# Kernel optimization log

Measured on AMD Instinct MI355X. Metric: run time of the kernel, lower is better.

## Reference

```python
import jax, jax.numpy as jnp
import numpy as np

N_EMBED = 1024
N_HEAD = 16
BLOCK_SIZE = 2048
ROPE_BASE = 10000.0


def _rope_cache():
    # theta uses n_embed (full model dim) as denominator, as in the source,
    # then is truncated to head_size//2 frequencies.
    hs_half = N_EMBED // N_HEAD // 2
    j = jnp.arange(N_EMBED // 2, dtype=jnp.float32)
    theta = jnp.power(ROPE_BASE, -2.0 * j / N_EMBED)
    seq_idx = jnp.arange(BLOCK_SIZE, dtype=jnp.float32)
    idx_theta = jnp.einsum('i,j->ij', seq_idx, theta)[:, :hs_half]  # [block, hs/2]
    return jnp.stack([jnp.cos(idx_theta), jnp.sin(idx_theta)], axis=-1)  # [block, hs/2, 2]


def _apply_rope(x, cache):
    # x: [B, nh, T, hs]. FAITHFUL to source: rope indexes its cache by dim-1,
    # which here is the HEAD dim (rope is called after transpose(1,2)).
    B, d1, d2, hs = x.shape
    rc = cache[:d1, :hs // 2]            # [d1, hs/2, 2]
    rc = rc[None, :, None, :, :]          # [1, d1, 1, hs/2, 2]
    x2 = x.reshape(B, d1, d2, hs // 2, 2)
    cos, sin = rc[..., 0], rc[..., 1]
    xr, xi = x2[..., 0], x2[..., 1]
    rot = jnp.stack([xr * cos - xi * sin, xi * cos + xr * sin], axis=-1)
    return rot.reshape(B, d1, d2, hs).astype(x.dtype)


def setup_inputs() -> dict:
    key = jax.random.key(0)
    ks = jax.random.split(key, 5)
    B, T, C = 2, 2048, N_EMBED
    return {
        'x': jax.random.normal(ks[0], (B, T, C), dtype=jnp.float32),
        'w_attn': jax.random.normal(ks[1], (C, 3 * C), dtype=jnp.float32) * 0.02,
        'b_attn': jax.random.normal(ks[2], (3 * C,), dtype=jnp.float32) * 0.02,
        'w_proj': jax.random.normal(ks[3], (C, C), dtype=jnp.float32) * 0.02,
        'b_proj': jax.random.normal(ks[4], (C,), dtype=jnp.float32) * 0.02,
    }


def reference(x, w_attn, b_attn, w_proj, b_proj):
    B, T, C = x.shape
    nh, hs = N_HEAD, C // N_HEAD
    qkv = x @ w_attn + b_attn                     # [B, T, 3C]
    q, k, v = jnp.split(qkv, 3, axis=-1)
    q = q.reshape(B, T, nh, hs).transpose(0, 2, 1, 3)  # [B, nh, T, hs]
    k = k.reshape(B, T, nh, hs).transpose(0, 2, 1, 3)
    v = v.reshape(B, T, nh, hs).transpose(0, 2, 1, 3)
    cache = _rope_cache()
    q = _apply_rope(q, cache)
    k = _apply_rope(k, cache)
    scale = 1.0 / jnp.sqrt(jnp.asarray(hs, dtype=q.dtype))
    scores = jnp.einsum('bhqd,bhkd->bhqk', q, k) * scale
    causal = jnp.tril(jnp.ones((T, T), dtype=bool))
    scores = jnp.where(causal[None, None], scores, jnp.finfo(scores.dtype).min)
    attn = jax.nn.softmax(scores, axis=-1)
    y = jnp.einsum('bhqk,bhkd->bhqd', attn, v)    # [B, nh, T, hs]
    y = y.transpose(0, 2, 1, 3).reshape(B, T, C)
    return y @ w_proj + b_proj
```

## Files before the change

### kernel.cpp

```cpp
#include <hip/hip_runtime.h>
#include <hip/hip_bf16.h>
#include <math.h>

#define TSEQ 2048
#define CEMB 1024
#define NHEAD 16
#define HS 64

typedef __attribute__((ext_vector_type(8))) short bf16x8;
typedef __attribute__((ext_vector_type(4))) float f32x4;
typedef __attribute__((ext_vector_type(16))) float f32x16;
typedef unsigned int u32;
typedef unsigned long long u64;
typedef unsigned short u16;

__device__ __forceinline__ void gload16(const void* g, void* l) {
    __builtin_amdgcn_global_load_lds(
        (const __attribute__((address_space(1))) unsigned int*)g,
        (__attribute__((address_space(3))) unsigned int*)l, 16, 0, 0);
}

__device__ __forceinline__ u32 pk2(float a, float b) {
    union { u32 u; __hip_bfloat16 h[2]; } t;
    t.h[0] = __float2bfloat16(a); t.h[1] = __float2bfloat16(b);
    return t.u;
}

__device__ __forceinline__ u16 bf16u(float a) {
    union { u16 u; __hip_bfloat16 h; } t;
    t.h = __float2bfloat16(a);
    return t.u;
}

__device__ const int UNIT_TBL[24] = {22,7,20,21,19,17,6,14,
                                     23,18,16,12,4,5,13,15,
                                     0,1,2,3,10,8,9,11};

__device__ __forceinline__ void transpose_tile(const float* __restrict__ src,
                                               __hip_bfloat16* __restrict__ dst,
                                               int K, int N, int n0, int k0) {
    __shared__ float tile[32][33];
    int tx = threadIdx.x & 31, ty = threadIdx.x >> 5;
#pragma unroll
    for (int i = 0; i < 32; i += 8)
        tile[ty + i][tx] = src[(size_t)(k0 + ty + i) * N + n0 + tx];
    __syncthreads();
#pragma unroll
    for (int i = 0; i < 32; i += 8)
        dst[(size_t)(n0 + ty + i) * K + k0 + tx] = __float2bfloat16(tile[tx][ty + i]);
}

__global__ __launch_bounds__(256) void prep_k(
    const float* __restrict__ x, __hip_bfloat16* __restrict__ Xb,
    float* __restrict__ tbl,
    const float* __restrict__ w_attn, __hip_bfloat16* __restrict__ Wta,
    const float* __restrict__ w_proj, __hip_bfloat16* __restrict__ Wpt)
{
    const int id = blockIdx.x;
    if (id < 2048) {
        int i = (id * 256 + threadIdx.x) * 8;
        float4 a = *(const float4*)(x + i);
        float4 b = *(const float4*)(x + i + 4);
        union { bf16x8 v; __hip_bfloat16 h[8]; } pk;
        pk.h[0] = __float2bfloat16(a.x); pk.h[1] = __float2bfloat16(a.y);
        pk.h[2] = __float2bfloat16(a.z); pk.h[3] = __float2bfloat16(a.w);
        pk.h[4] = __float2bfloat16(b.x); pk.h[5] = __float2bfloat16(b.y);
        pk.h[6] = __float2bfloat16(b.z); pk.h[7] = __float2bfloat16(b.w);
        *(bf16x8*)(Xb + i) = pk.v;
    } else if (id == 2048) {
#pragma unroll
        for (int it = 0; it < 2; ++it) {
            int idx = threadIdx.x + 256 * it;
            int h = idx >> 5, j = idx & 31;
            double theta = pow(10000.0, -2.0 * (double)j / 1024.0);
            double ang = (double)h * theta;
            tbl[2 * idx + 0] = (float)cos(ang);
            tbl[2 * idx + 1] = (float)sin(ang);
        }
    } else if (id < 2049 + 3072) {
        int t = id - 2049;
        transpose_tile(w_attn, Wta, CEMB, 3 * CEMB, (t % 96) * 32, (t / 96) * 32);
    } else {
        int t = id - (2049 + 3072);
        transpose_tile(w_proj, Wpt, CEMB, CEMB, (t & 31) * 32, (t >> 5) * 32);
    }
}

__global__ __launch_bounds__(256) void qkv_mfma_k(
    const __hip_bfloat16* __restrict__ Xb, const __hip_bfloat16* __restrict__ Wt,
    const float* __restrict__ bias, const float* __restrict__ tbl,
    __hip_bfloat16* __restrict__ Qb, __hip_bfloat16* __restrict__ Kb,
    __hip_bfloat16* __restrict__ Vtb)
{
    __shared__ __hip_bfloat16 SM[4][128 * 32];
    const int tid = threadIdx.x;
    const int lane = tid & 63, w = tid >> 6;
    const int lr = lane & 15, lg = lane >> 4;
    const int wm = w >> 1, wn = w & 1;
    const int n0 = blockIdx.x * 128;
    const int m0 = blockIdx.y * 128;
    const __hip_bfloat16* gA = Xb + (size_t)(m0 + (tid >> 2)) * CEMB + (tid & 3) * 8;
    const __hip_bfloat16* gB = Wt + (size_t)(n0 + (tid >> 2)) * CEMB + (tid & 3) * 8;
#define QSTAGE(buf, kk) do { \
        gload16(gA + (kk), &SM[buf][tid * 8]); \
        gload16(gA + 64 * CEMB + (kk), &SM[buf][2048 + tid * 8]); \
        gload16(gB + (kk), &SM[2 + (buf)][tid * 8]); \
        gload16(gB + 64 * CEMB + (kk), &SM[2 + (buf)][2048 + tid * 8]); } while (0)
    f32x4 acc[4][4] = {};
    QSTAGE(0, 0);
    __syncthreads();
    for (int k0 = 0; k0 < CEMB; k0 += 32) {
        const int cur = (k0 >> 5) & 1;
        if (k0 + 32 < CEMB) QSTAGE(cur ^ 1, k0 + 32);
        bf16x8 af[4], bfr[4];
#pragma unroll
        for (int mi = 0; mi < 4; ++mi)
            af[mi] = *(const bf16x8*)&SM[cur][(wm * 64 + mi * 16 + lr) * 32 + lg * 8];
#pragma unroll
        for (int ni = 0; ni < 4; ++ni)
            bfr[ni] = *(const bf16x8*)&SM[2 + cur][(wn * 64 + ni * 16 + lr) * 32 + lg * 8];
#pragma unroll
        for (int mi = 0; mi < 4; ++mi)
#pragma unroll
            for (int ni = 0; ni < 4; ++ni)
                acc[mi][ni] = __builtin_amdgcn_mfma_f32_16x16x32_bf16(af[mi], bfr[ni], acc[mi][ni], 0, 0, 0);
        __syncthreads();
    }
    const int sec = (n0 >> 10);
    const int bb = m0 >> 11;
    const int t0v = m0 & 2047;
    const int h0 = (n0 & 1023) >> 6;
    if (sec == 2) {
        char* T = (char*)SM;
#pragma unroll
        for (int mi = 0; mi < 4; ++mi) {
#pragma unroll
            for (int ni = 0; ni < 4; ++ni) {
                const int nl = wn * 64 + ni * 16 + lr;
                const float bv = bias[n0 + nl];
                const int mb = wm * 64 + mi * 16 + lg * 4;
                union { u64 u; __hip_bfloat16 hh[4]; } pk;
#pragma unroll
                for (int r = 0; r < 4; ++r) pk.hh[r] = __float2bfloat16(acc[mi][ni][r] + bv);
                *(u64*)(T + nl * 256 + ((mb * 2) ^ ((nl & 7) << 4))) = pk.u;
            }
        }
        __syncthreads();
#pragma unroll
        for (int i = 0; i < 8; ++i) {
            int cid = tid + 256 * i;
            int n = cid >> 4, mc = cid & 15;
            bf16x8 v = *(const bf16x8*)(T + n * 256 + ((mc * 16) ^ ((n & 7) << 4)));
            *(bf16x8*)&Vtb[(((size_t)bb * NHEAD + h0 + (n >> 6)) * HS + (n & 63)) * TSEQ + t0v + mc * 8] = v;
        }
    } else {
        char* T = (char*)SM;
        const float sc = (sec == 0) ? 0.18033688011112042f : 1.0f;
        __hip_bfloat16* dst = (sec == 0) ? Qb : Kb;
#pragma unroll
        for (int mi = 0; mi < 4; ++mi) {
#pragma unroll
            for (int ni = 0; ni < 4; ++ni) {
                const int nl = wn * 64 + ni * 16 + lr;
                const int c63 = (n0 + nl) & 63;
                const int h = h0 + (nl >> 6);
                const int j = c63 >> 1;
                const float cth = tbl[(h * 32 + j) * 2 + 0];
                const float sth = tbl[(h * 32 + j) * 2 + 1];
                const float bv = bias[n0 + nl];
                const int mb = wm * 64 + mi * 16 + lg * 4;
#pragma unroll
                for (int r = 0; r < 4; ++r) {
                    float val = acc[mi][ni][r] + bv;
                    float prt = __shfl_xor(val, 1);
                    float rot = (lr & 1) ? (val * cth + prt * sth) : (val * cth - prt * sth);
                    const int row = mb + r;
                    *(u16*)(T + row * 256 + ((nl * 2) ^ ((row & 7) << 4))) = bf16u(rot * sc);
                }
            }
        }
        __syncthreads();
#pragma unroll
        for (int i = 0; i < 8; ++i) {
            int cid = tid + 256 * i;
            int row = cid >> 4, nc = cid & 15;
            bf16x8 v = *(const bf16x8*)(T + row * 256 + ((nc * 16) ^ ((row & 7) << 4)));
            int col = nc * 8;
            *(bf16x8*)&dst[(((size_t)bb * NHEAD + h0 + (col >> 6)) * TSEQ + t0v + row) * HS + (col & 63)] = v;
        }
    }
#undef QSTAGE
}

__global__ __launch_bounds__(256) void attn_split_k(
    const __hip_bfloat16* __restrict__ Q, const __hip_bfloat16* __restrict__ K,
    const __hip_bfloat16* __restrict__ Vt, __hip_bfloat16* __restrict__ Y,
    __hip_bfloat16* __restrict__ Op, float* __restrict__ Mp, float* __restrict__ Lp)
{
    __shared__ __hip_bfloat16 KsBuf[2][64 * 64];
    __shared__ __hip_bfloat16 VsBuf[2][64 * 64];
    const int tid = threadIdx.x;
    const int w = tid >> 6;
    const int lane = tid & 63;
    const int l31 = lane & 31;
    const int hi = lane >> 5;
    const int id = blockIdx.x;
    const int bh = id & 31;
    const int u = UNIT_TBL[id >> 5];
    int qbb, kt0, ktN, half;
    bool split;
    if (u < 8) { qbb = u; half = 0; kt0 = 0; ktN = 2 * u + 2; split = false; }
    else {
        qbb = 8 + ((u - 8) >> 1); half = (u - 8) & 1;
        kt0 = half ? (qbb + 1) : 0;
        ktN = half ? (2 * qbb + 2) : (qbb + 1);
        split = true;
    }
    const size_t bho = (size_t)bh * TSEQ * HS;
    const int Qw = qbb * 128 + w * 32;

    int srcK[2], srcV[2];
#pragma unroll
    for (int j = 0; j < 2; ++j) {
        int L = (tid + 256 * j) * 16;
        int row = L >> 7;
        int ce = ((L & 127) ^ (((row ^ (row >> 3)) & 7) << 4)) >> 1;
        srcK[j] = row * HS + ce;
        srcV[j] = row * TSEQ + ce;
    }
    const __hip_bfloat16* Kg = K + bho;
    const __hip_bfloat16* Vg = Vt + bho;
#define ASTAGE(buf, kt_) do { \
        const __hip_bfloat16* kg_ = Kg + (size_t)(kt_) * 64 * HS; \
        const __hip_bfloat16* vg_ = Vg + (size_t)(kt_) * 64; \
        char* kb_ = (char*)KsBuf[buf]; char* vb_ = (char*)VsBuf[buf]; \
        _Pragma("unroll") \
        for (int j = 0; j < 2; ++j) { \
            gload16(kg_ + srcK[j], kb_ + (tid + 256 * j) * 16); \
            gload16(vg_ + srcV[j], vb_ + (tid + 256 * j) * 16); } } while (0)

    bf16x8 qf[4];
    {
        const __hip_bfloat16* qp = Q + bho + (size_t)(Qw + l31) * HS + hi * 8;
#pragma unroll
        for (int kb = 0; kb < 4; ++kb) qf[kb] = *(const bf16x8*)(qp + kb * 16);
    }
    const int base0 = l31 * 128;
    const int swz0 = ((l31 ^ (l31 >> 3)) & 7) << 4;
    const int r32 = 32 + l31;
    const int base1 = r32 * 128;
    const int swz1 = ((r32 ^ (r32 >> 3)) & 7) << 4;

    float mrow = -1e30f, lsum = 0.f;
    f32x16 o0 = {}, o1 = {};

    ASTAGE(0, kt0);
    __syncthreads();
    for (int kt = kt0; kt < ktN; ++kt) {
        const int cur = (kt - kt0) & 1;
        if (kt + 1 < ktN) ASTAGE(cur ^ 1, kt + 1);
        const char* KsB = (const char*)KsBuf[cur];
        const char* VsB = (const char*)VsBuf[cur];
        const int kvb0 = kt * 64, kvb1 = kt * 64 + 32;
        const bool do0 = kvb0 <= Qw;
        const bool do1 = kvb1 <= Qw;
        if (do0) {
            f32x16 s0 = {}, s1 = {};
            __builtin_amdgcn_s_setprio(1);
#pragma unroll
            for (int kb = 0; kb < 4; ++kb) {
                bf16x8 kf = *(const bf16x8*)(KsB + base0 + ((kb * 32 + hi * 16) ^ swz0));
                s0 = __builtin_amdgcn_mfma_f32_32x32x16_bf16(kf, qf[kb], s0, 0, 0, 0);
            }
            if (do1) {
#pragma unroll
                for (int kb = 0; kb < 4; ++kb) {
                    bf16x8 kf = *(const bf16x8*)(KsB + base1 + ((kb * 32 + hi * 16) ^ swz1));
                    s1 = __builtin_amdgcn_mfma_f32_32x32x16_bf16(kf, qf[kb], s1, 0, 0, 0);
                }
            }
            __builtin_amdgcn_s_setprio(0);
            if (kvb0 == Qw) {
#pragma unroll
                for (int r = 0; r < 16; ++r) {
                    int crow = (r & 3) + 8 * (r >> 2) + 4 * hi;
                    if (crow > l31) s0[r] = -1e30f;
                }
            }
            if (do1 && kvb1 == Qw) {
#pragma unroll
                for (int r = 0; r < 16; ++r) {
                    int crow = (r & 3) + 8 * (r >> 2) + 4 * hi;
                    if (crow > l31) s1[r] = -1e30f;
                }
            }
            float mx = s0[0];
#pragma unroll
            for (int r = 1; r < 16; ++r) mx = fmaxf(mx, s0[r]);
            if (do1) {
#pragma unroll
                for (int r = 0; r < 16; ++r) mx = fmaxf(mx, s1[r]);
            }
            mx = fmaxf(mx, __shfl_xor(mx, 32));
            const float mn = fmaxf(mrow, mx);
            const float alpha = __builtin_amdgcn_exp2f(mrow - mn);
            mrow = mn;
            float ls = 0.f;
#pragma unroll
            for (int r = 0; r < 16; ++r) { s0[r] = __builtin_amdgcn_exp2f(s0[r] - mn); ls += s0[r]; }
            if (do1) {
#pragma unroll
                for (int r = 0; r < 16; ++r) { s1[r] = __builtin_amdgcn_exp2f(s1[r] - mn); ls += s1[r]; }
            }
            ls += __shfl_xor(ls, 32);
            lsum = lsum * alpha + ls;
            o0 = o0 * alpha;
            o1 = o1 * alpha;
            union { u32 u[4]; bf16x8 v; } pa[4];
            {
                u32 w01 = pk2(s0[0], s0[1]),   w23 = pk2(s0[2], s0[3]);
                u32 w45 = pk2(s0[4], s0[5]),   w67 = pk2(s0[6], s0[7]);
                u32 w89 = pk2(s0[8], s0[9]),   wab = pk2(s0[10], s0[11]);
                u32 wcd = pk2(s0[12], s0[13]), wef = pk2(s0[14], s0[15]);
                u32 xa = __shfl_xor(hi ? w01 : w45, 32);
                u32 xb = __shfl_xor(hi ? w23 : w67, 32);
                u32 xc = __shfl_xor(hi ? w89 : wcd, 32);
                u32 xd = __shfl_xor(hi ? wab : wef, 32);
                if (hi == 0) {
                    pa[0].u[0] = w01; pa[0].u[1] = w23; pa[0].u[2] = xa;  pa[0].u[3] = xb;
                    pa[1].u[0] = w89; pa[1].u[1] = wab; pa[1].u[2] = xc;  pa[1].u[3] = xd;
                } else {
                    pa[0].u[0] = xa;  pa[0].u[1] = xb;  pa[0].u[2] = w45; pa[0].u[3] = w67;
                    pa[1].u[0] = xc;  pa[1].u[1] = xd;  pa[1].u[2] = wcd; pa[1].u[3] = wef;
                }
            }
            if (do1) {
                u32 w01 = pk2(s1[0], s1[1]),   w23 = pk2(s1[2], s1[3]);
                u32 w45 = pk2(s1[4], s1[5]),   w67 = pk2(s1[6], s1[7]);
                u32 w89 = pk2(s1[8], s1[9]),   wab = pk2(s1[10], s1[11]);
                u32 wcd = pk2(s1[12], s1[13]), wef = pk2(s1[14], s1[15]);
                u32 xa = __shfl_xor(hi ? w01 : w45, 32);
                u32 xb = __shfl_xor(hi ? w23 : w67, 32);
                u32 xc = __shfl_xor(hi ? w89 : wcd, 32);
                u32 xd = __shfl_xor(hi ? wab : wef, 32);
                if (hi == 0) {
                    pa[2].u[0] = w01; pa[2].u[1] = w23; pa[2].u[2] = xa;  pa[2].u[3] = xb;
                    pa[3].u[0] = w89; pa[3].u[1] = wab; pa[3].u[2] = xc;  pa[3].u[3] = xd;
                } else {
                    pa[2].u[0] = xa;  pa[2].u[1] = xb;  pa[2].u[2] = w45; pa[2].u[3] = w67;
                    pa[3].u[0] = xc;  pa[3].u[1] = xd;  pa[3].u[2] = wcd; pa[3].u[3] = wef;
                }
            }
            __builtin_amdgcn_s_setprio(1);
#define PVC(ks) do { \
                bf16x8 vf0 = *(const bf16x8*)(VsB + base0 + (((ks) * 32 + hi * 16) ^ swz0)); \
                o0 = __builtin_amdgcn_mfma_f32_32x32x16_bf16(vf0, pa[ks].v, o0, 0, 0, 0); \
                bf16x8 vf1 = *(const bf16x8*)(VsB + base1 + (((ks) * 32 + hi * 16) ^ swz1)); \
                o1 = __builtin_amdgcn_mfma_f32_32x32x16_bf16(vf1, pa[ks].v, o1, 0, 0, 0); } while (0)
            PVC(0); PVC(1);
            if (do1) { PVC(2); PVC(3); }
#undef PVC
            __builtin_amdgcn_s_setprio(0);
        }
        __syncthreads();
    }
    if (!split) {
        char* T = (char*)KsBuf + w * 4096;
        const float inv = 1.f / lsum;
        const int tsw = (l31 & 7) << 4;
        const int tbase = l31 * 128;
#pragma unroll
        for (int r = 0; r < 16; ++r) {
            int d0 = (r & 3) + 8 * (r >> 2) + 4 * hi;
            *(__hip_bfloat16*)(T + tbase + ((d0 * 2) ^ tsw)) = __float2bfloat16(o0[r] * inv);
            *(__hip_bfloat16*)(T + tbase + (((d0 + 32) * 2) ^ tsw)) = __float2bfloat16(o1[r] * inv);
        }
        const int b = bh >> 4, h = bh & 15;
#pragma unroll
        for (int p = 0; p < 4; ++p) {
            int q = p * 8 + (lane >> 3);
            int colb = ((lane & 7) * 16) ^ ((q & 7) << 4);
            bf16x8 v = *(const bf16x8*)(T + q * 128 + colb);
            *(bf16x8*)(Y + ((size_t)b * TSEQ + Qw + q) * CEMB + h * HS + (lane & 7) * 8) = v;
        }
    } else {
        const int p = bh * 16 + (qbb - 8) * 2 + half;
        __hip_bfloat16* Ob = Op + (size_t)p * 8192;
        const int qloc = w * 32 + l31;
#pragma unroll
        for (int r = 0; r < 16; ++r) {
            int d0 = (r & 3) + 8 * (r >> 2) + 4 * hi;
            Ob[d0 * 128 + qloc] = __float2bfloat16(o0[r]);
            Ob[(d0 + 32) * 128 + qloc] = __float2bfloat16(o1[r]);
        }
        if (hi == 0) {
            Mp[p * 128 + qloc] = mrow;
            Lp[p * 128 + qloc] = lsum;
        }
    }
#undef ASTAGE
}

__global__ __launch_bounds__(256) void merge_k(
    const __hip_bfloat16* __restrict__ Op, const float* __restrict__ Mp,
    const float* __restrict__ Lp, __hip_bfloat16* __restrict__ Y)
{
    const int blk = blockIdx.x;
    const int bh = blk & 31, qq = blk >> 5;
    const int p0 = bh * 16 + qq * 2, p1 = p0 + 1;
    const int t = threadIdx.x;
    const int q = t >> 1, dg = (t & 1) * 32;
    const float m0 = Mp[p0 * 128 + q], m1 = Mp[p1 * 128 + q];
    const float l0 = Lp[p0 * 128 + q], l1 = Lp[p1 * 128 + q];
    const float m = fmaxf(m0, m1);
    const float w0 = exp2f(m0 - m), w1 = exp2f(m1 - m);
    const float inv = 1.f / (l0 * w0 + l1 * w1);
    const __hip_bfloat16* O0 = Op + (size_t)p0 * 8192;
    const __hip_bfloat16* O1 = Op + (size_t)p1 * 8192;
    union { bf16x8 v[4]; __hip_bfloat16 h[32]; } outp;
#pragma unroll
    for (int i = 0; i < 32; ++i) {
        int d = dg + i;
        float a = __bfloat162float(O0[d * 128 + q]);
        float b = __bfloat162float(O1[d * 128 + q]);
        outp.h[i] = __float2bfloat16((a * w0 + b * w1) * inv);
    }
    const int b2 = bh >> 4, h = bh & 15;
    const int qg = (8 + qq) * 128 + q;
    __hip_bfloat16* yp = Y + ((size_t)b2 * TSEQ + qg) * CEMB + h * HS + dg;
#pragma unroll
    for (int i = 0; i < 4; ++i) *(bf16x8*)(yp + i * 8) = outp.v[i];
}

__global__ __launch_bounds__(256) void proj_mfma_k(
    const __hip_bfloat16* __restrict__ Ab, const __hip_bfloat16* __restrict__ Wt,
    const float* __restrict__ bias, float* __restrict__ out)
{
    __shared__ __hip_bfloat16 Al[2][128 * 32];
    __shared__ __hip_bfloat16 Bl[2][64 * 32];
    const int tid = threadIdx.x;
    const int lane = tid & 63, w = tid >> 6;
    const int lr = lane & 15, lg = lane >> 4;
    const int wm = w >> 1, wn = w & 1;
    const int n0 = blockIdx.x * 64;
    const int m0 = blockIdx.y * 128;
    const __hip_bfloat16* gA = Ab + (size_t)(m0 + (tid >> 2)) * CEMB + (tid & 3) * 8;
    const __hip_bfloat16* gB = Wt + (size_t)(n0 + (tid >> 2)) * CEMB + (tid & 3) * 8;
#define PSTAGE(buf, kk) do { \
        gload16(gA + (kk), &Al[buf][tid * 8]); \
        gload16(gA + 64 * CEMB + (kk), &Al[buf][2048 + tid * 8]); \
        gload16(gB + (kk), &Bl[buf][tid * 8]); } while (0)
    f32x4 acc[4][2] = {};
    PSTAGE(0, 0);
    __syncthreads();
    for (int k0 = 0; k0 < CEMB; k0 += 32) {
        const int cur = (k0 >> 5) & 1;
        if (k0 + 32 < CEMB) PSTAGE(cur ^ 1, k0 + 32);
        bf16x8 af[4], bfr[2];
#pragma unroll
        for (int mi = 0; mi < 4; ++mi)
            af[mi] = *(const bf16x8*)&Al[cur][(wm * 64 + mi * 16 + lr) * 32 + lg * 8];
#pragma unroll
        for (int ni = 0; ni < 2; ++ni)
            bfr[ni] = *(const bf16x8*)&Bl[cur][(wn * 32 + ni * 16 + lr) * 32 + lg * 8];
#pragma unroll
        for (int mi = 0; mi < 4; ++mi)
#pragma unroll
            for (int ni = 0; ni < 2; ++ni)
                acc[mi][ni] = __builtin_amdgcn_mfma_f32_16x16x32_bf16(af[mi], bfr[ni], acc[mi][ni], 0, 0, 0);
        __syncthreads();
    }
#pragma unroll
    for (int mi = 0; mi < 4; ++mi) {
#pragma unroll
        for (int ni = 0; ni < 2; ++ni) {
            const int gcol = n0 + wn * 32 + ni * 16 + lr;
            const float bv = bias[gcol];
            const int growb = m0 + wm * 64 + mi * 16 + lg * 4;
#pragma unroll
            for (int r = 0; r < 4; ++r)
                out[(size_t)(growb + r) * CEMB + gcol] = acc[mi][ni][r] + bv;
        }
    }
#undef PSTAGE
}

extern "C" void kernel_launch(void* const* d_in, const int* in_sizes, int n_in,
                              void* d_out, int out_size, void* d_ws, size_t ws_size,
                              hipStream_t stream)
{
    const float* x      = (const float*)d_in[0];
    const float* w_attn = (const float*)d_in[1];
    const float* b_attn = (const float*)d_in[2];
    const float* w_proj = (const float*)d_in[3];
    const float* b_proj = (const float*)d_in[4];
    float* out = (float*)d_out;
    char* base = (char*)d_ws;

    const size_t MB = 1048576;
    float* tbl          = (float*)base;
    __hip_bfloat16* Xb  = (__hip_bfloat16*)(base + 4096);
    __hip_bfloat16* Wta = (__hip_bfloat16*)(base + 4096 + 8 * MB);
    __hip_bfloat16* Wpt = (__hip_bfloat16*)(base + 4096 + 14 * MB);
    __hip_bfloat16* Qb  = (__hip_bfloat16*)(base + 4096 + 16 * MB);
    __hip_bfloat16* Kb  = (__hip_bfloat16*)(base + 4096 + 24 * MB);
    __hip_bfloat16* Vtb = (__hip_bfloat16*)(base + 4096 + 32 * MB);
    __hip_bfloat16* Yb  = Xb;
    const size_t PART_OFF = 4096 + 40 * MB;
    __hip_bfloat16* Op = (__hip_bfloat16*)(base + PART_OFF);
    float* Mp = (float*)(base + PART_OFF + 8 * MB);
    float* Lp = Mp + (size_t)512 * 128;

    prep_k<<<6145, 256, 0, stream>>>(x, Xb, tbl, w_attn, Wta, w_proj, Wpt);
    qkv_mfma_k<<<dim3(24, 32), 256, 0, stream>>>(Xb, Wta, b_attn, tbl, Qb, Kb, Vtb);
    attn_split_k<<<768, 256, 0, stream>>>(Qb, Kb, Vtb, Yb, Op, Mp, Lp);
    merge_k<<<256, 256, 0, stream>>>(Op, Mp, Lp, Yb);
    proj_mfma_k<<<dim3(16, 32), 256, 0, stream>>>(Yb, Wpt, b_proj, out);
}
```

Measured before the change: 121.3 us.

## Fuse split-KV merge into attention kernel using last-arriver atomic flags

Removes the separate merge kernel launch. Each split attention block writes its partial output, fences, and atomically increments a per-pair counter, and the second block to arrive merges both partials and writes Y. Flags are reset in the prep kernel. This saves one launch and its tail, at the cost of extra fences and syncs, plus a serialized merge inside the last block of each pair.

```diff
diff --git a/kernel.cpp b/kernel.cpp
--- a/kernel.cpp
+++ b/kernel.cpp
@@ -54,7 +54,8 @@
     const float* __restrict__ x, __hip_bfloat16* __restrict__ Xb,
     float* __restrict__ tbl,
     const float* __restrict__ w_attn, __hip_bfloat16* __restrict__ Wta,
-    const float* __restrict__ w_proj, __hip_bfloat16* __restrict__ Wpt)
+    const float* __restrict__ w_proj, __hip_bfloat16* __restrict__ Wpt,
+    int* __restrict__ flags)
 {
     const int id = blockIdx.x;
     if (id < 2048) {
@@ -68,6 +69,7 @@
         pk.h[6] = __float2bfloat16(b.z); pk.h[7] = __float2bfloat16(b.w);
         *(bf16x8*)(Xb + i) = pk.v;
     } else if (id == 2048) {
+        flags[threadIdx.x] = 0;
 #pragma unroll
         for (int it = 0; it < 2; ++it) {
             int idx = threadIdx.x + 256 * it;
@@ -195,7 +197,8 @@
 __global__ __launch_bounds__(256) void attn_split_k(
     const __hip_bfloat16* __restrict__ Q, const __hip_bfloat16* __restrict__ K,
     const __hip_bfloat16* __restrict__ Vt, __hip_bfloat16* __restrict__ Y,
-    __hip_bfloat16* __restrict__ Op, float* __restrict__ Mp, float* __restrict__ Lp)
+    __hip_bfloat16* __restrict__ Op, float* __restrict__ Mp, float* __restrict__ Lp,
+    int* __restrict__ flags)
 {
     __shared__ __hip_bfloat16 KsBuf[2][64 * 64];
     __shared__ __hip_bfloat16 VsBuf[2][64 * 64];
@@ -397,39 +400,39 @@
             Mp[p * 128 + qloc] = mrow;
             Lp[p * 128 + qloc] = lsum;
         }
+        __syncthreads();
+        __threadfence();
+        __syncthreads();
+        int* sflag = (int*)KsBuf;
+        if (tid == 0) sflag[0] = atomicAdd(&flags[p >> 1], 1);
+        __syncthreads();
+        if (sflag[0] == 1) {
+            __threadfence();
+            const int p0 = (p >> 1) << 1, p1 = p0 + 1;
+            const int q = tid >> 1, dg = (tid & 1) * 32;
+            const float m0 = Mp[p0 * 128 + q], m1 = Mp[p1 * 128 + q];
+            const float l0 = Lp[p0 * 128 + q], l1 = Lp[p1 * 128 + q];
+            const float m = fmaxf(m0, m1);
+            const float w0 = exp2f(m0 - m), w1 = exp2f(m1 - m);
+            const float inv = 1.f / (l0 * w0 + l1 * w1);
+            const __hip_bfloat16* O0 = Op + (size_t)p0 * 8192;
+            const __hip_bfloat16* O1 = Op + (size_t)p1 * 8192;
+            union { bf16x8 v[4]; __hip_bfloat16 hh[32]; } outp;
+#pragma unroll
+            for (int i = 0; i < 32; ++i) {
+                int d = dg + i;
+                float a = __bfloat162float(O0[d * 128 + q]);
+                float b = __bfloat162float(O1[d * 128 + q]);
+                outp.hh[i] = __float2bfloat16((a * w0 + b * w1) * inv);
+            }
+            const int b2 = bh >> 4, h = bh & 15;
+            const int qg = qbb * 128 + q;
+            __hip_bfloat16* yp = Y + ((size_t)b2 * TSEQ + qg) * CEMB + h * HS + dg;
+#pragma unroll
+            for (int i = 0; i < 4; ++i) *(bf16x8*)(yp + i * 8) = outp.v[i];
+        }
     }
 #undef ASTAGE
-}
-
-__global__ __launch_bounds__(256) void merge_k(
-    const __hip_bfloat16* __restrict__ Op, const float* __restrict__ Mp,
-    const float* __restrict__ Lp, __hip_bfloat16* __restrict__ Y)
-{
-    const int blk = blockIdx.x;
-    const int bh = blk & 31, qq = blk >> 5;
-    const int p0 = bh * 16 + qq * 2, p1 = p0 + 1;
-    const int t = threadIdx.x;
-    const int q = t >> 1, dg = (t & 1) * 32;
-    const float m0 = Mp[p0 * 128 + q], m1 = Mp[p1 * 128 + q];
-    const float l0 = Lp[p0 * 128 + q], l1 = Lp[p1 * 128 + q];
-    const float m = fmaxf(m0, m1);
-    const float w0 = exp2f(m0 - m), w1 = exp2f(m1 - m);
-    const float inv = 1.f / (l0 * w0 + l1 * w1);
-    const __hip_bfloat16* O0 = Op + (size_t)p0 * 8192;
-    const __hip_bfloat16* O1 = Op + (size_t)p1 * 8192;
-    union { bf16x8 v[4]; __hip_bfloat16 h[32]; } outp;
-#pragma unroll
-    for (int i = 0; i < 32; ++i) {
-        int d = dg + i;
-        float a = __bfloat162float(O0[d * 128 + q]);
-        float b = __bfloat162float(O1[d * 128 + q]);
-        outp.h[i] = __float2bfloat16((a * w0 + b * w1) * inv);
-    }
-    const int b2 = bh >> 4, h = bh & 15;
-    const int qg = (8 + qq) * 128 + q;
-    __hip_bfloat16* yp = Y + ((size_t)b2 * TSEQ + qg) * CEMB + h * HS + dg;
-#pragma unroll
-    for (int i = 0; i < 4; ++i) *(bf16x8*)(yp + i * 8) = outp.v[i];
 }
 
 __global__ __launch_bounds__(256) void proj_mfma_k(
@@ -510,10 +513,10 @@
     __hip_bfloat16* Op = (__hip_bfloat16*)(base + PART_OFF);
     float* Mp = (float*)(base + PART_OFF + 8 * MB);
     float* Lp = Mp + (size_t)512 * 128;
-
-    prep_k<<<6145, 256, 0, stream>>>(x, Xb, tbl, w_attn, Wta, w_proj, Wpt);
+    int* flags = (int*)(Lp + (size_t)512 * 128);
+
+    prep_k<<<6145, 256, 0, stream>>>(x, Xb, tbl, w_attn, Wta, w_proj, Wpt, flags);
     qkv_mfma_k<<<dim3(24, 32), 256, 0, stream>>>(Xb, Wta, b_attn, tbl, Qb, Kb, Vtb);
-    attn_split_k<<<768, 256, 0, stream>>>(Qb, Kb, Vtb, Yb, Op, Mp, Lp);
-    merge_k<<<256, 256, 0, stream>>>(Op, Mp, Lp, Yb);
+    attn_split_k<<<768, 256, 0, stream>>>(Qb, Kb, Vtb, Yb, Op, Mp, Lp, flags);
     proj_mfma_k<<<dim3(16, 32), 256, 0, stream>>>(Yb, Wpt, b_proj, out);
 }
```

New measurement: 204.9 us. +68.9%, slower.
